# Optimization experiments

Hardware: AMD Instinct MI355X
Metric: run time of the kernel (lower is better)

## Reference

```python
import jax, jax.numpy as jnp
import numpy as np

N, D, E = 65536, 64, 4096


def setup_inputs() -> dict:
    key = jax.random.key(0)
    k1, k2, k3 = jax.random.split(key, 3)
    return {
        "input_data": jax.random.normal(k1, (N, D), dtype=jnp.float32),
        "codebook": jax.random.normal(k2, (E, D), dtype=jnp.float32),
        "dither": jax.random.uniform(k3, (E - 1,), dtype=jnp.float32),
        "entries": E,
    }


def _decode(frac_idx, cb):
    # linear interpolation between consecutive codebook entries
    e = cb.shape[0]
    ii = jnp.clip(jnp.floor(frac_idx), 0, e - 2).astype(jnp.int32)
    r = (frac_idx - ii.astype(frac_idx.dtype))[..., None]
    return (1.0 - r) * cb[ii] + r * cb[ii + 1]


def reference(input_data, codebook, dither, entries):
    cur = codebook[:entries]                                   # (E, D)
    # fractional_index = dither + linspace(0, E-2, E-1) == dither + arange(E-1)
    frac = dither + jnp.arange(entries - 1, dtype=dither.dtype)
    dithered_cb = _decode(frac, cur)                           # (E-1, D)
    # squared euclidean distances via expansion (same argmin as (x-c)^2 sum)
    x2 = jnp.sum(input_data * input_data, axis=1, keepdims=True)   # (N, 1)
    c2 = jnp.sum(dithered_cb * dithered_cb, axis=1)                # (E-1,)
    dist = x2 - 2.0 * (input_data @ dithered_cb.T) + c2[None, :]   # (N, E-1)
    integer_index = jnp.argmin(dist, axis=1)                       # (N,)
    quantized = _decode(integer_index.astype(input_data.dtype), dithered_cb)
    # perplexity = exp(entropy of codebook usage) over `entries` bins
    counts = jnp.zeros((entries,), dtype=jnp.float32).at[integer_index].add(1.0)
    avg_probs = counts / input_data.shape[0]
    perplexity = jnp.exp(-jnp.sum(avg_probs * jnp.log(avg_probs + 1e-10)))
    return quantized, perplexity, integer_index
```

## Files before the change

### kernel.cpp

```cpp
#include <hip/hip_runtime.h>
#include <math.h>


constexpr int D = 64;
constexpr int CHUNK = 64;
constexpr int NTILES = CHUNK / 16;
constexpr int E_PAD = 4096;
constexpr int ESLICES = 2;
constexpr int SLICE = E_PAD / ESLICES;
constexpr int NCH = SLICE / CHUNK;
constexpr float TAU = 0.005f;
constexpr int BLK = 256;

typedef __attribute__((ext_vector_type(8))) short bf16x8;
typedef __attribute__((ext_vector_type(4))) float f32x4;

__device__ inline unsigned short f2bf(float x) {
  unsigned int u = __float_as_uint(x);
  u = (u + 0x7fffu + ((u >> 16) & 1u)) >> 16;
  return (unsigned short)u;
}
__device__ inline float bf2f(unsigned short h) {
  return __uint_as_float(((unsigned int)h) << 16);
}

__device__ __forceinline__ void gll16(const void* g, void* l) {
  __builtin_amdgcn_global_load_lds(
      (const __attribute__((address_space(1))) unsigned int*)g,
      (__attribute__((address_space(3))) unsigned int*)l, 16, 0, 0);
}
__device__ __forceinline__ void gll4(const void* g, void* l) {
  __builtin_amdgcn_global_load_lds(
      (const __attribute__((address_space(1))) unsigned int*)g,
      (__attribute__((address_space(3))) unsigned int*)l, 4, 0, 0);
}

__global__ __launch_bounds__(256) void build_kernel(
    const float* __restrict__ cb, const float* __restrict__ dither,
    float* __restrict__ dcb, unsigned short* __restrict__ dcbh,
    unsigned short* __restrict__ dcbl, float* __restrict__ c2h,
    float* __restrict__ counts, int* __restrict__ rescue_n, int E, int Em1) {
  int i = blockIdx.x * 4 + (threadIdx.x >> 6);
  int k = threadIdx.x & 63;
  if (k == 0) counts[i] = 0.0f;
  if (i == 0 && k == 1) *rescue_n = 0;
  if (i >= Em1) {
    dcb[(size_t)i * D + k] = 0.f;
    dcbh[(size_t)i * D + k] = 0;
    dcbl[(size_t)i * D + k] = 0;
    if (k == 0) c2h[i] = 3.0e38f;
    return;
  }
  float frac = dither[i] + (float)i;
  int ii = (int)floorf(frac);
  ii = max(0, min(ii, E - 2));
  float r = frac - (float)ii;
  float v = (1.0f - r) * cb[(size_t)ii * D + k] + r * cb[(size_t)(ii + 1) * D + k];
  dcb[(size_t)i * D + k] = v;
  unsigned short h = f2bf(v);
  unsigned short l = f2bf(v - bf2f(h));
  dcbh[(size_t)i * D + k] = h;
  dcbl[(size_t)i * D + k] = l;
  float s = v * v;
#pragma unroll
  for (int off = 32; off > 0; off >>= 1) s += __shfl_down(s, off, 64);
  if (k == 0) c2h[i] = 0.5f * s;
}

__global__ __launch_bounds__(BLK, 4) void vq_mfma_kernel(
    const float* __restrict__ X, const unsigned short* __restrict__ dcbh,
    const unsigned short* __restrict__ dcbl, const float* __restrict__ c2h,
    float* __restrict__ out_b1, int* __restrict__ out_i1,
    float* __restrict__ out_b2, int N) {
  __shared__ unsigned short s_h[2][CHUNK * D];
  __shared__ unsigned short s_l[2][CHUNK * D];
  __shared__ float s_c2[2][CHUNK];

  const int tid = threadIdx.x;
  const int lane = tid & 63;
  const int wv = tid >> 6;
  const int col = lane & 15;
  const int kg = lane >> 4;
  const int slice = blockIdx.y;
  const int sbase = slice * SLICE;
  const int wvbase = blockIdx.x * 128 + wv * 32;

  bf16x8 ah0[2], ah1[2], al0[2], al1[2];
#pragma unroll
  for (int rg = 0; rg < 2; ++rg) {
    const float* xp = X + (size_t)(wvbase + rg * 16 + col) * D + kg * 8;
#pragma unroll
    for (int i = 0; i < 8; ++i) {
      float x0 = xp[i], x1 = xp[32 + i];
      unsigned short h0 = f2bf(x0), h1 = f2bf(x1);
      ah0[rg][i] = (short)h0; ah1[rg][i] = (short)h1;
      al0[rg][i] = (short)f2bf(x0 - bf2f(h0));
      al1[rg][i] = (short)f2bf(x1 - bf2f(h1));
    }
  }

  float b1[2][4], b2[2][4];
  int i1[2][4];
#pragma unroll
  for (int rg = 0; rg < 2; ++rg)
#pragma unroll
    for (int r = 0; r < 4; ++r) { b1[rg][r] = -3.4e38f; b2[rg][r] = -3.4e38f; i1[rg][r] = sbase; }

  const int xs = col & 7;

  auto stage = [&](int ch, int buf) {
#pragma unroll
    for (int i = 0; i < 2; ++i) {
      const int u = (wv * 2 + i) * 64 + lane;
      const int e = u >> 3, g = u & 7;
      const size_t goff = (((size_t)(sbase + ch * CHUNK + e)) << 6) + ((g ^ (e & 7)) << 3);
      char* dst_h = (char*)s_h[buf] + (size_t)(wv * 2 + i) * 1024;
      char* dst_l = (char*)s_l[buf] + (size_t)(wv * 2 + i) * 1024;
      gll16(dcbh + goff, dst_h);
      gll16(dcbl + goff, dst_l);
    }
    if (wv == 0) {
      gll4(c2h + sbase + ch * CHUNK + lane, (char*)s_c2[buf]);
    }
  };

  stage(0, 0);
  __syncthreads();
  int cur = 0;

  for (int ch = 0; ch < NCH; ++ch) {
    const int ebase = sbase + ch * CHUNK;
    if (ch + 1 < NCH) stage(ch + 1, cur ^ 1);

#pragma unroll
    for (int p = 0; p < 2; ++p) {
      bf16x8 Bh0[2], Bh1[2], Bl0[2], Bl1[2];
      float hc2[2];
#pragma unroll
      for (int q = 0; q < 2; ++q) {
        const int el = (p * 2 + q) * 16 + col;
        const char* bb = (const char*)s_h[cur] + el * 128;
        const char* ll = (const char*)s_l[cur] + el * 128;
        Bh0[q] = *(const bf16x8*)(bb + ((kg ^ xs) << 4));
        Bh1[q] = *(const bf16x8*)(bb + (((kg + 4) ^ xs) << 4));
        Bl0[q] = *(const bf16x8*)(ll + ((kg ^ xs) << 4));
        Bl1[q] = *(const bf16x8*)(ll + (((kg + 4) ^ xs) << 4));
        hc2[q] = s_c2[cur][el];
      }
      f32x4 acc[2][2];
#pragma unroll
      for (int q = 0; q < 2; ++q)
#pragma unroll
        for (int rg = 0; rg < 2; ++rg)
          acc[q][rg] = {-hc2[q], -hc2[q], -hc2[q], -hc2[q]};
      __builtin_amdgcn_s_setprio(1);
#pragma unroll
      for (int q = 0; q < 2; ++q)
#pragma unroll
        for (int rg = 0; rg < 2; ++rg) {
          acc[q][rg] = __builtin_amdgcn_mfma_f32_16x16x32_bf16(ah0[rg], Bh0[q], acc[q][rg], 0, 0, 0);
          acc[q][rg] = __builtin_amdgcn_mfma_f32_16x16x32_bf16(ah1[rg], Bh1[q], acc[q][rg], 0, 0, 0);
          acc[q][rg] = __builtin_amdgcn_mfma_f32_16x16x32_bf16(ah0[rg], Bl0[q], acc[q][rg], 0, 0, 0);
          acc[q][rg] = __builtin_amdgcn_mfma_f32_16x16x32_bf16(ah1[rg], Bl1[q], acc[q][rg], 0, 0, 0);
          acc[q][rg] = __builtin_amdgcn_mfma_f32_16x16x32_bf16(al0[rg], Bh0[q], acc[q][rg], 0, 0, 0);
          acc[q][rg] = __builtin_amdgcn_mfma_f32_16x16x32_bf16(al1[rg], Bh1[q], acc[q][rg], 0, 0, 0);
        }
      __builtin_amdgcn_s_setprio(0);
#pragma unroll
      for (int q = 0; q < 2; ++q) {
        const int colg = ebase + (p * 2 + q) * 16 + col;
#pragma unroll
        for (int rg = 0; rg < 2; ++rg)
#pragma unroll
          for (int r = 0; r < 4; ++r) {
            float s = acc[q][rg][r];
            bool gt = s > b1[rg][r];
            b2[rg][r] = __builtin_amdgcn_fmed3f(b2[rg][r], s, b1[rg][r]);
            b1[rg][r] = fmaxf(b1[rg][r], s);
            i1[rg][r] = gt ? colg : i1[rg][r];
          }
      }
    }

    __syncthreads();
    cur ^= 1;
  }

#pragma unroll
  for (int m = 1; m < 16; m <<= 1) {
#pragma unroll
    for (int rg = 0; rg < 2; ++rg)
#pragma unroll
      for (int r = 0; r < 4; ++r) {
        float ob1 = __shfl_xor(b1[rg][r], m, 64);
        float ob2 = __shfl_xor(b2[rg][r], m, 64);
        int oi1 = __shfl_xor(i1[rg][r], m, 64);
        float loser = fminf(b1[rg][r], ob1);
        b2[rg][r] = fmaxf(fmaxf(b2[rg][r], ob2), loser);
        bool take = (ob1 > b1[rg][r]) || (ob1 == b1[rg][r] && oi1 < i1[rg][r]);
        b1[rg][r] = take ? ob1 : b1[rg][r];
        i1[rg][r] = take ? oi1 : i1[rg][r];
      }
  }
  if (col == 0) {
#pragma unroll
    for (int rg = 0; rg < 2; ++rg)
#pragma unroll
      for (int r = 0; r < 4; ++r) {
        int row = wvbase + rg * 16 + kg * 4 + r;
        size_t o = (size_t)slice * N + row;
        out_b1[o] = b1[rg][r];
        out_i1[o] = i1[rg][r];
        out_b2[o] = b2[rg][r];
      }
  }
}

__global__ __launch_bounds__(64) void finish_kernel(
    const float* __restrict__ out_b1, const int* __restrict__ out_i1,
    const float* __restrict__ out_b2,
    const float* __restrict__ dcb, float* __restrict__ outq,
    float* __restrict__ outidx, float* __restrict__ counts,
    int* __restrict__ rescue_n, int* __restrict__ rescue_list, int N) {
  __shared__ int s_idx[64];
  const int lane = threadIdx.x;
  const int rowbase = blockIdx.x * 64;
  const int row = rowbase + lane;

  float b1c = out_b1[row];
  int bi = out_i1[row];
  float b2c = out_b2[row];
#pragma unroll
  for (int k = 1; k < ESLICES; ++k) {
    float sk = out_b1[(size_t)k * N + row];
    int ek = out_i1[(size_t)k * N + row];
    float qk = out_b2[(size_t)k * N + row];
    b2c = fmaxf(fmaxf(b2c, qk), fminf(sk, b1c));
    bool take = sk > b1c;
    b1c = take ? sk : b1c;
    bi = take ? ek : bi;
  }
  float gap2 = 2.0f * (b1c - b2c);

  outidx[row] = (float)bi;
  s_idx[lane] = bi;
  if (gap2 < TAU) {
    int p = atomicAdd(rescue_n, 1);
    rescue_list[p] = row;
  } else {
    atomicAdd(&counts[bi], 1.0f);
  }
  __syncthreads();

  const f32x4* dcb4 = (const f32x4*)dcb;
  f32x4* outq4 = (f32x4*)outq;
  const int rl = lane >> 4;
  const int c4 = lane & 15;
#pragma unroll 4
  for (int t = 0; t < 16; ++t) {
    const int rloc = t * 4 + rl;
    const int idx = s_idx[rloc];
    f32x4 v = dcb4[(size_t)idx * 16 + c4];
    __builtin_nontemporal_store(v, &outq4[(size_t)(rowbase + rloc) * 16 + c4]);
  }
}

__global__ __launch_bounds__(256) void rescue_kernel(
    const float* __restrict__ X, const float* __restrict__ dcb,
    const float* __restrict__ c2h, const int* __restrict__ rescue_n,
    const int* __restrict__ rescue_list, float* __restrict__ outq,
    float* __restrict__ outidx, float* __restrict__ counts, int Em1) {
  __shared__ float sx[D];
  __shared__ float sd[4];
  __shared__ int si[4];
  __shared__ int sbest;
  const int tid = threadIdx.x;
  const int nr = *rescue_n;
  for (int li = blockIdx.x; li < nr; li += gridDim.x) {
    const int row = rescue_list[li];
    __syncthreads();
    if (tid < D) sx[tid] = X[(size_t)row * D + tid];
    __syncthreads();

    float best = 3.4e38f;
    int bidx = 0x7fffffff;
    for (int e = tid; e < Em1; e += 256) {
      const float4* cp = (const float4*)(dcb + (size_t)e * D);
      float d0 = 0.f, d1 = 0.f, d2 = 0.f, d3 = 0.f;
#pragma unroll
      for (int k = 0; k < 16; ++k) {
        float4 c = cp[k];
        d0 = fmaf(sx[k * 4 + 0], c.x, d0);
        d1 = fmaf(sx[k * 4 + 1], c.y, d1);
        d2 = fmaf(sx[k * 4 + 2], c.z, d2);
        d3 = fmaf(sx[k * 4 + 3], c.w, d3);
      }
      float d = c2h[e] - ((d0 + d1) + (d2 + d3));
      if (d < best) { best = d; bidx = e; }
    }
#pragma unroll
    for (int m = 1; m < 64; m <<= 1) {
      float od = __shfl_xor(best, m, 64);
      int oi = __shfl_xor(bidx, m, 64);
      if (od < best || (od == best && oi < bidx)) { best = od; bidx = oi; }
    }
    if ((tid & 63) == 0) { sd[tid >> 6] = best; si[tid >> 6] = bidx; }
    __syncthreads();
    if (tid == 0) {
      float bb = sd[0]; int bi2 = si[0];
      for (int w = 1; w < 4; ++w)
        if (sd[w] < bb || (sd[w] == bb && si[w] < bi2)) { bb = sd[w]; bi2 = si[w]; }
      sbest = bi2;
      outidx[row] = (float)bi2;
      atomicAdd(&counts[bi2], 1.0f);
    }
    __syncthreads();
    const int bfin = sbest;
    if (tid < D) outq[(size_t)row * D + tid] = dcb[(size_t)bfin * D + tid];
  }
}

__global__ __launch_bounds__(256) void vq_perp_kernel(
    const float* __restrict__ counts, float* __restrict__ out, int E, float invN) {
  __shared__ float red[4];
  float s = 0.f;
  for (int j = threadIdx.x; j < E; j += 256) {
    float p = counts[j] * invN;
    s += p * logf(p + 1e-10f);
  }
#pragma unroll
  for (int off = 32; off > 0; off >>= 1) s += __shfl_down(s, off, 64);
  int wid = threadIdx.x >> 6;
  if ((threadIdx.x & 63) == 0) red[wid] = s;
  __syncthreads();
  if (threadIdx.x == 0) {
    float t = (red[0] + red[1]) + (red[2] + red[3]);
    out[0] = expf(-t);
  }
}

static inline size_t align256(size_t x) { return (x + 255) & ~(size_t)255; }

extern "C" void kernel_launch(void* const* d_in, const int* in_sizes, int n_in,
                              void* d_out, int out_size, void* d_ws, size_t ws_size,
                              hipStream_t stream) {
  const float* X      = (const float*)d_in[0];
  const float* cb     = (const float*)d_in[1];
  const float* dither = (const float*)d_in[2];

  const int N   = in_sizes[0] / D;
  const int E   = in_sizes[1] / D;
  const int Em1 = in_sizes[2];

  char* w = (char*)d_ws;
  float* dcb            = (float*)w;          w += align256((size_t)E_PAD * D * sizeof(float));
  unsigned short* dcbh  = (unsigned short*)w; w += align256((size_t)E_PAD * D * sizeof(short));
  unsigned short* dcbl  = (unsigned short*)w; w += align256((size_t)E_PAD * D * sizeof(short));
  float* c2h            = (float*)w;          w += align256((size_t)E_PAD * sizeof(float));
  float* out_b1         = (float*)w;          w += align256((size_t)ESLICES * N * sizeof(float));
  int* out_i1           = (int*)w;            w += align256((size_t)ESLICES * N * sizeof(int));
  float* out_b2         = (float*)w;          w += align256((size_t)ESLICES * N * sizeof(float));
  float* counts         = (float*)w;          w += align256((size_t)E_PAD * sizeof(float));
  int* rescue_n         = (int*)w;            w += align256(sizeof(int));
  int* rescue_list      = (int*)w;            w += align256((size_t)N * sizeof(int));

  float* outq   = (float*)d_out;
  float* perp   = (float*)d_out + (size_t)N * D;
  float* outidx = (float*)d_out + (size_t)N * D + 1;

  build_kernel<<<E_PAD / 4, 256, 0, stream>>>(cb, dither, dcb, dcbh, dcbl, c2h,
                                              counts, rescue_n, E, Em1);

  dim3 g2(N / 128, ESLICES);
  vq_mfma_kernel<<<g2, BLK, 0, stream>>>(X, dcbh, dcbl, c2h, out_b1, out_i1, out_b2, N);

  finish_kernel<<<N / 64, 64, 0, stream>>>(out_b1, out_i1, out_b2, dcb, outq, outidx,
                                           counts, rescue_n, rescue_list, N);

  rescue_kernel<<<2048, 256, 0, stream>>>(X, dcb, c2h, rescue_n, rescue_list,
                                          outq, outidx, counts, Em1);

  vq_perp_kernel<<<1, 256, 0, stream>>>(counts, perp, E, 1.0f / (float)N);
}
```

Measured before the change: 163.7 us.

## Switch distance GEMM to 32x32x16 MFMA tiles with 512-thread blocks

Replaces the 16x16x32 bf16 MFMA tiling (each wave covering 32 rows in two 16-row groups) with a single 32x32x16 MFMA tile per 32-entry column group, using 16 accumulator registers per lane. Blocks grow to 512 threads covering 256 rows, so each staged codebook chunk in LDS is shared by more waves and each wave issues one 16-byte global-to-LDS load per buffer. The intent is to cut LDS traffic for B fragments and instruction overhead per FLOP. The cost is more registers for the running argmax state and a longer cross-lane reduction over 32 lanes, and the explicit occupancy hint in launch_bounds is removed.

```diff
diff --git a/kernel.cpp b/kernel.cpp
--- a/kernel.cpp
+++ b/kernel.cpp
@@ -4,16 +4,17 @@
 
 constexpr int D = 64;
 constexpr int CHUNK = 64;
-constexpr int NTILES = CHUNK / 16;
 constexpr int E_PAD = 4096;
 constexpr int ESLICES = 2;
 constexpr int SLICE = E_PAD / ESLICES;
 constexpr int NCH = SLICE / CHUNK;
 constexpr float TAU = 0.005f;
-constexpr int BLK = 256;
+constexpr int BLK = 512;
+constexpr int ROWS_PER_BLOCK = 256;
 
 typedef __attribute__((ext_vector_type(8))) short bf16x8;
 typedef __attribute__((ext_vector_type(4))) float f32x4;
+typedef __attribute__((ext_vector_type(16))) float f32x16;
 
 __device__ inline unsigned short f2bf(float x) {
   unsigned int u = __float_as_uint(x);
@@ -67,7 +68,7 @@
   if (k == 0) c2h[i] = 0.5f * s;
 }
 
-__global__ __launch_bounds__(BLK, 4) void vq_mfma_kernel(
+__global__ __launch_bounds__(BLK) void vq_mfma_kernel(
     const float* __restrict__ X, const unsigned short* __restrict__ dcbh,
     const unsigned short* __restrict__ dcbl, const float* __restrict__ c2h,
     float* __restrict__ out_b1, int* __restrict__ out_i1,
@@ -79,46 +80,39 @@
   const int tid = threadIdx.x;
   const int lane = tid & 63;
   const int wv = tid >> 6;
-  const int col = lane & 15;
-  const int kg = lane >> 4;
+  const int col = lane & 31;
+  const int kh = lane >> 5;
   const int slice = blockIdx.y;
   const int sbase = slice * SLICE;
-  const int wvbase = blockIdx.x * 128 + wv * 32;
-
-  bf16x8 ah0[2], ah1[2], al0[2], al1[2];
-#pragma unroll
-  for (int rg = 0; rg < 2; ++rg) {
-    const float* xp = X + (size_t)(wvbase + rg * 16 + col) * D + kg * 8;
-#pragma unroll
-    for (int i = 0; i < 8; ++i) {
-      float x0 = xp[i], x1 = xp[32 + i];
-      unsigned short h0 = f2bf(x0), h1 = f2bf(x1);
-      ah0[rg][i] = (short)h0; ah1[rg][i] = (short)h1;
-      al0[rg][i] = (short)f2bf(x0 - bf2f(h0));
-      al1[rg][i] = (short)f2bf(x1 - bf2f(h1));
-    }
-  }
-
-  float b1[2][4], b2[2][4];
-  int i1[2][4];
-#pragma unroll
-  for (int rg = 0; rg < 2; ++rg)
-#pragma unroll
-    for (int r = 0; r < 4; ++r) { b1[rg][r] = -3.4e38f; b2[rg][r] = -3.4e38f; i1[rg][r] = sbase; }
+  const int wvbase = blockIdx.x * ROWS_PER_BLOCK + wv * 32;
+
+  bf16x8 ah[4], al[4];
+  {
+    const float* xp = X + (size_t)(wvbase + col) * D + kh * 8;
+#pragma unroll
+    for (int s = 0; s < 4; ++s)
+#pragma unroll
+      for (int i = 0; i < 8; ++i) {
+        float x = xp[s * 16 + i];
+        unsigned short h = f2bf(x);
+        ah[s][i] = (short)h;
+        al[s][i] = (short)f2bf(x - bf2f(h));
+      }
+  }
+
+  float b1[16], b2[16];
+  int i1[16];
+#pragma unroll
+  for (int r = 0; r < 16; ++r) { b1[r] = -3.4e38f; b2[r] = -3.4e38f; i1[r] = sbase; }
 
   const int xs = col & 7;
 
   auto stage = [&](int ch, int buf) {
-#pragma unroll
-    for (int i = 0; i < 2; ++i) {
-      const int u = (wv * 2 + i) * 64 + lane;
-      const int e = u >> 3, g = u & 7;
-      const size_t goff = (((size_t)(sbase + ch * CHUNK + e)) << 6) + ((g ^ (e & 7)) << 3);
-      char* dst_h = (char*)s_h[buf] + (size_t)(wv * 2 + i) * 1024;
-      char* dst_l = (char*)s_l[buf] + (size_t)(wv * 2 + i) * 1024;
-      gll16(dcbh + goff, dst_h);
-      gll16(dcbl + goff, dst_l);
-    }
+    const int u = wv * 64 + lane;
+    const int e = u >> 3, g = u & 7;
+    const size_t goff = (((size_t)(sbase + ch * CHUNK + e)) << 6) + ((g ^ (e & 7)) << 3);
+    gll16(dcbh + goff, (char*)s_h[buf] + (size_t)wv * 1024);
+    gll16(dcbl + goff, (char*)s_l[buf] + (size_t)wv * 1024);
     if (wv == 0) {
       gll4(c2h + sbase + ch * CHUNK + lane, (char*)s_c2[buf]);
     }
@@ -133,52 +127,36 @@
     if (ch + 1 < NCH) stage(ch + 1, cur ^ 1);
 
 #pragma unroll
-    for (int p = 0; p < 2; ++p) {
-      bf16x8 Bh0[2], Bh1[2], Bl0[2], Bl1[2];
-      float hc2[2];
-#pragma unroll
-      for (int q = 0; q < 2; ++q) {
-        const int el = (p * 2 + q) * 16 + col;
-        const char* bb = (const char*)s_h[cur] + el * 128;
-        const char* ll = (const char*)s_l[cur] + el * 128;
-        Bh0[q] = *(const bf16x8*)(bb + ((kg ^ xs) << 4));
-        Bh1[q] = *(const bf16x8*)(bb + (((kg + 4) ^ xs) << 4));
-        Bl0[q] = *(const bf16x8*)(ll + ((kg ^ xs) << 4));
-        Bl1[q] = *(const bf16x8*)(ll + (((kg + 4) ^ xs) << 4));
-        hc2[q] = s_c2[cur][el];
+    for (int t = 0; t < 2; ++t) {
+      const int el = t * 32 + col;
+      const float hc2 = s_c2[cur][el];
+      const int colg = ebase + el;
+      const char* bb = (const char*)s_h[cur] + el * 128;
+      const char* ll = (const char*)s_l[cur] + el * 128;
+
+      f32x16 acc;
+#pragma unroll
+      for (int r = 0; r < 16; ++r) acc[r] = -hc2;
+
+      __builtin_amdgcn_s_setprio(1);
+#pragma unroll
+      for (int s = 0; s < 4; ++s) {
+        const int g = kh + 2 * s;
+        bf16x8 Bh = *(const bf16x8*)(bb + ((g ^ xs) << 4));
+        bf16x8 Bl = *(const bf16x8*)(ll + ((g ^ xs) << 4));
+        acc = __builtin_amdgcn_mfma_f32_32x32x16_bf16(ah[s], Bh, acc, 0, 0, 0);
+        acc = __builtin_amdgcn_mfma_f32_32x32x16_bf16(ah[s], Bl, acc, 0, 0, 0);
+        acc = __builtin_amdgcn_mfma_f32_32x32x16_bf16(al[s], Bh, acc, 0, 0, 0);
       }
-      f32x4 acc[2][2];
-#pragma unroll
-      for (int q = 0; q < 2; ++q)
-#pragma unroll
-        for (int rg = 0; rg < 2; ++rg)
-          acc[q][rg] = {-hc2[q], -hc2[q], -hc2[q], -hc2[q]};
-      __builtin_amdgcn_s_setprio(1);
-#pragma unroll
-      for (int q = 0; q < 2; ++q)
-#pragma unroll
-        for (int rg = 0; rg < 2; ++rg) {
-          acc[q][rg] = __builtin_amdgcn_mfma_f32_16x16x32_bf16(ah0[rg], Bh0[q], acc[q][rg], 0, 0, 0);
-          acc[q][rg] = __builtin_amdgcn_mfma_f32_16x16x32_bf16(ah1[rg], Bh1[q], acc[q][rg], 0, 0, 0);
-          acc[q][rg] = __builtin_amdgcn_mfma_f32_16x16x32_bf16(ah0[rg], Bl0[q], acc[q][rg], 0, 0, 0);
-          acc[q][rg] = __builtin_amdgcn_mfma_f32_16x16x32_bf16(ah1[rg], Bl1[q], acc[q][rg], 0, 0, 0);
-          acc[q][rg] = __builtin_amdgcn_mfma_f32_16x16x32_bf16(al0[rg], Bh0[q], acc[q][rg], 0, 0, 0);
-          acc[q][rg] = __builtin_amdgcn_mfma_f32_16x16x32_bf16(al1[rg], Bh1[q], acc[q][rg], 0, 0, 0);
-        }
       __builtin_amdgcn_s_setprio(0);
-#pragma unroll
-      for (int q = 0; q < 2; ++q) {
-        const int colg = ebase + (p * 2 + q) * 16 + col;
-#pragma unroll
-        for (int rg = 0; rg < 2; ++rg)
-#pragma unroll
-          for (int r = 0; r < 4; ++r) {
-            float s = acc[q][rg][r];
-            bool gt = s > b1[rg][r];
-            b2[rg][r] = __builtin_amdgcn_fmed3f(b2[rg][r], s, b1[rg][r]);
-            b1[rg][r] = fmaxf(b1[rg][r], s);
-            i1[rg][r] = gt ? colg : i1[rg][r];
-          }
+
+#pragma unroll
+      for (int r = 0; r < 16; ++r) {
+        float sv = acc[r];
+        bool gt = sv > b1[r];
+        b2[r] = __builtin_amdgcn_fmed3f(b2[r], sv, b1[r]);
+        b1[r] = fmaxf(b1[r], sv);
+        i1[r] = gt ? colg : i1[r];
       }
     }
 
@@ -187,32 +165,28 @@
   }
 
 #pragma unroll
-  for (int m = 1; m < 16; m <<= 1) {
-#pragma unroll
-    for (int rg = 0; rg < 2; ++rg)
-#pragma unroll
-      for (int r = 0; r < 4; ++r) {
-        float ob1 = __shfl_xor(b1[rg][r], m, 64);
-        float ob2 = __shfl_xor(b2[rg][r], m, 64);
-        int oi1 = __shfl_xor(i1[rg][r], m, 64);
-        float loser = fminf(b1[rg][r], ob1);
-        b2[rg][r] = fmaxf(fmaxf(b2[rg][r], ob2), loser);
-        bool take = (ob1 > b1[rg][r]) || (ob1 == b1[rg][r] && oi1 < i1[rg][r]);
-        b1[rg][r] = take ? ob1 : b1[rg][r];
-        i1[rg][r] = take ? oi1 : i1[rg][r];
-      }
+  for (int m = 1; m < 32; m <<= 1) {
+#pragma unroll
+    for (int r = 0; r < 16; ++r) {
+      float ob1 = __shfl_xor(b1[r], m, 64);
+      float ob2 = __shfl_xor(b2[r], m, 64);
+      int oi1 = __shfl_xor(i1[r], m, 64);
+      float loser = fminf(b1[r], ob1);
+      b2[r] = fmaxf(fmaxf(b2[r], ob2), loser);
+      bool take = (ob1 > b1[r]) || (ob1 == b1[r] && oi1 < i1[r]);
+      b1[r] = take ? ob1 : b1[r];
+      i1[r] = take ? oi1 : i1[r];
+    }
   }
   if (col == 0) {
 #pragma unroll
-    for (int rg = 0; rg < 2; ++rg)
-#pragma unroll
-      for (int r = 0; r < 4; ++r) {
-        int row = wvbase + rg * 16 + kg * 4 + r;
-        size_t o = (size_t)slice * N + row;
-        out_b1[o] = b1[rg][r];
-        out_i1[o] = i1[rg][r];
-        out_b2[o] = b2[rg][r];
-      }
+    for (int r = 0; r < 16; ++r) {
+      int row = wvbase + (r & 3) + 8 * (r >> 2) + 4 * kh;
+      size_t o = (size_t)slice * N + row;
+      out_b1[o] = b1[r];
+      out_i1[o] = i1[r];
+      out_b2[o] = b2[r];
+    }
   }
 }
 
@@ -371,7 +345,7 @@
   build_kernel<<<E_PAD / 4, 256, 0, stream>>>(cb, dither, dcb, dcbh, dcbl, c2h,
                                               counts, rescue_n, E, Em1);
 
-  dim3 g2(N / 128, ESLICES);
+  dim3 g2(N / ROWS_PER_BLOCK, ESLICES);
   vq_mfma_kernel<<<g2, BLK, 0, stream>>>(X, dcbh, dcbl, c2h, out_b1, out_i1, out_b2, N);
 
   finish_kernel<<<N / 64, 64, 0, stream>>>(out_b1, out_i1, out_b2, dcb, outq, outidx,
```

Result: slower. 192.6 us (+17.7%).
